# Kernel tuning notes

Hardware: AMD Instinct MI355X
Metric: run time of the kernel (lower is better)

The kernel has to match this reference:

```python
import jax, jax.numpy as jnp
import numpy as np

B, S, N, U, A = 256, 24, 207, 64, 256
H = N * U  # hidden_state_size = num_nodes * rnn_units


def setup_inputs() -> dict:
    key = jax.random.key(0)
    ks = jax.random.split(key, 9)
    return {
        "inputs": jax.random.normal(ks[0], (B, N), dtype=jnp.float32),
        "encoder_outputs": jax.random.normal(ks[1], (S, B, H), dtype=jnp.float32),
        "hidden_state": jax.random.normal(ks[2], (1, B, H), dtype=jnp.float32) * 0.05,
        "adj": jax.random.uniform(ks[3], (N, N), dtype=jnp.float32) / N,
        "attn_W": jax.random.normal(ks[4], (2 * H, A), dtype=jnp.float32) * 0.01,
        "attn_b": jnp.zeros((A,), dtype=jnp.float32),
        "attn_v": jax.random.normal(ks[5], (A,), dtype=jnp.float32) * 0.1,
        "W_ru": jax.random.normal(ks[6], (1 + 2 * U, 2 * U), dtype=jnp.float32) * 0.1,
        "b_ru": jnp.zeros((2 * U,), dtype=jnp.float32),
        "W_c": jax.random.normal(ks[7], (1 + 2 * U, U), dtype=jnp.float32) * 0.1,
        "b_c": jnp.zeros((U,), dtype=jnp.float32),
        "proj_W": jax.random.normal(ks[8], (2 * U + 1, 1), dtype=jnp.float32) * 0.1,
        "proj_b": jnp.zeros((1,), dtype=jnp.float32),
    }


def reference(inputs, encoder_outputs, hidden_state, adj, attn_W, attn_b, attn_v,
              W_ru, b_ru, W_c, b_c, proj_W, proj_b):
    b = inputs.shape[0]
    hid = hidden_state[-1]                               # (B, H) top-layer decoder state
    enc = jnp.transpose(encoder_outputs, (1, 0, 2))      # (B, S, H)

    # Bahdanau attention: tanh(Linear(cat(hid, enc))) . v, softmax over src_len.
    # Split the weight so we never materialize the (B, S, 2H) concat.
    Wh, We = attn_W[:H], attn_W[H:]
    energy = jnp.tanh((hid @ Wh)[:, None, :] + jnp.einsum('bsh,ha->bsa', enc, We) + attn_b)
    scores = energy @ attn_v                             # (B, S)
    a = jax.nn.softmax(scores, axis=1)
    weighted = jnp.einsum('bs,bsh->bh', a, enc).reshape(b, N, U)  # (B, N, U)

    # Graph-conv GRU cell (DCRNN-style), single layer.
    x = jnp.concatenate([inputs.reshape(b, N, 1), weighted], axis=-1)  # (B, N, 1+U)
    h = hid.reshape(b, N, U)
    m = jnp.einsum('nm,bmf->bnf', adj, jnp.concatenate([x, h], axis=-1))  # message passing
    ru = jax.nn.sigmoid(m @ W_ru + b_ru)                 # (B, N, 2U)
    r, u = ru[..., :U], ru[..., U:]
    mc = jnp.einsum('nm,bmf->bnf', adj, jnp.concatenate([x, r * h], axis=-1))
    c = jnp.tanh(mc @ W_c + b_c)                         # (B, N, U)
    new_h = u * h + (1.0 - u) * c                        # (B, N, U)

    # Projection: Linear(2U+1 -> 1) on per-node cat(output, weighted, inputs).
    proj_in = jnp.concatenate([new_h, weighted, inputs.reshape(b, N, 1)], axis=-1)
    output = (proj_in @ proj_W + proj_b).reshape(b, N)   # (B, N*output_dim)
    return output, new_h.reshape(1, b, H)
```

## Files before the change

kernel.cpp:

```cpp
#include <hip/hip_runtime.h>
#include <hip/hip_bf16.h>
#include <math.h>

#define B_ 256
#define S_ 24
#define N_ 207
#define U_ 64
#define A_ 256
#define H_ (N_*U_)
#define H2_ (2*H_)
#define BS_ (B_*S_)
#define NF_ 129
#define FP_ 192
#define KP_ 256
#define MR_ 6400
#define ZSPL_ 9

typedef __attribute__((ext_vector_type(8))) short bf16x8;
typedef __attribute__((ext_vector_type(4))) float f32x4;

#define GAS __attribute__((address_space(1)))
#define LAS __attribute__((address_space(3)))

static __device__ __forceinline__ void gload16(const __hip_bfloat16* g, void* lds) {
    __builtin_amdgcn_global_load_lds((const GAS uint32_t*)g, (LAS uint32_t*)lds, 16, 0, 0);
}

template<int BM, int BN, int EPI>
__global__ __launch_bounds__(256)
void mfma_gemm(const __hip_bfloat16* __restrict__ A, int lda,
               const __hip_bfloat16* __restrict__ BT, int ldb,
               void* __restrict__ Cv, int ldc,
               int kchunk, int niter,
               const float* __restrict__ ep0,
               const float* __restrict__ ep1,
               const float* __restrict__ ep2,
               const float* __restrict__ e_wt,
               const float* __restrict__ e_pw,
               const float* __restrict__ e_pb,
               const float* __restrict__ e_in,
               float* __restrict__ e_o0)
{
    constexpr int FM = BM / 32, FN = BN / 32;
    __shared__ __align__(128) char smem[(BM + BN) * 128];
    char* As = smem;
    char* Bs = smem + BM * 128;

    const int tid  = threadIdx.x;
    const int lane = tid & 63;
    const int wid  = tid >> 6;
    const int wr   = wid >> 1, wc = wid & 1;

    const int n0 = blockIdx.x * BN;
    const int m0 = blockIdx.y * BM;
    const long k0 = (long)blockIdx.z * kchunk;

    const int qk = lane >> 4;
    const int fr = lane & 15;
    const int sw = (lane & 7) << 4;

    f32x4 acc[FM][FN] = {};

    for (int it = 0; it < niter; ++it) {
        const long kb = k0 + (long)it * 64;
        #pragma unroll
        for (int p = 0; p < BM / 32; ++p) {
            const int chunk = p * 4 + wid;
            const int blk   = chunk * 64 + lane;
            const int r     = blk >> 3;
            const int klog  = ((blk & 7) << 4) ^ ((r & 7) << 4);
            gload16(A + (size_t)(m0 + r) * lda + kb + (klog >> 1), As + chunk * 1024);
        }
        #pragma unroll
        for (int p = 0; p < BN / 32; ++p) {
            const int chunk = p * 4 + wid;
            const int blk   = chunk * 64 + lane;
            const int r     = blk >> 3;
            const int klog  = ((blk & 7) << 4) ^ ((r & 7) << 4);
            gload16(BT + (size_t)(n0 + r) * ldb + kb + (klog >> 1), Bs + chunk * 1024);
        }
        __syncthreads();
        #pragma unroll
        for (int ks = 0; ks < 2; ++ks) {
            const int ko = ks * 64 + qk * 16;
            bf16x8 a[FM], b[FN];
            #pragma unroll
            for (int i = 0; i < FM; ++i)
                a[i] = *(const bf16x8*)(As + (wr * (BM/2) + i * 16 + fr) * 128 + (ko ^ sw));
            #pragma unroll
            for (int j = 0; j < FN; ++j)
                b[j] = *(const bf16x8*)(Bs + (wc * (BN/2) + j * 16 + fr) * 128 + (ko ^ sw));
            #pragma unroll
            for (int i = 0; i < FM; ++i)
                #pragma unroll
                for (int j = 0; j < FN; ++j)
                    acc[i][j] = __builtin_amdgcn_mfma_f32_16x16x32_bf16(a[i], b[j], acc[i][j], 0, 0, 0);
        }
        __syncthreads();
    }

    float* rsum = (float*)smem;
    if (EPI == 5) {
        if (tid < BM) rsum[tid] = 0.f;
        __syncthreads();
    }
    float tpart[FM][4];
    if (EPI == 5) {
        #pragma unroll
        for (int mi = 0; mi < FM; ++mi)
            #pragma unroll
            for (int q = 0; q < 4; ++q) tpart[mi][q] = 0.f;
    }

    #pragma unroll
    for (int mi = 0; mi < FM; ++mi)
        #pragma unroll
        for (int ni = 0; ni < FN; ++ni) {
            const int rbase = m0 + wr * (BM/2) + mi * 16 + qk * 4;
            const int col   = n0 + wc * (BN/2) + ni * 16 + fr;
            #pragma unroll
            for (int q = 0; q < 4; ++q) {
                const int row = rbase + q;
                const float v = acc[mi][ni][q];
                if (EPI == 2) {
                    ((__hip_bfloat16*)Cv)[(size_t)row * ldc + col] = __float2bfloat16(v);
                } else if (EPI == 3) {
                    const int bb = col >> 6, uu = col & 63;
                    ((__hip_bfloat16*)Cv)[((size_t)row * 256 + bb) * FP_ + 65 + uu] = __float2bfloat16(v);
                } else if (EPI == 4) {
                    float sv = v + ep0[col];
                    ((float*)Cv)[(size_t)row * ldc + col] = 1.f / (1.f + expf(-sv));
                } else {
                    const int nn = row >> 8, bb = row & 255;
                    float cg = tanhf(v + ep0[col]);
                    float ug = ep1[(size_t)row * 128 + 64 + col];
                    const size_t hoff = (size_t)bb * H_ + nn * U_ + col;
                    float nh = ug * ep2[hoff] + (1.f - ug) * cg;
                    ((float*)Cv)[hoff] = nh;
                    tpart[mi][q] += nh * e_pw[col] + e_wt[hoff] * e_pw[64 + col];
                }
            }
        }

    if (EPI == 5) {
        #pragma unroll
        for (int mi = 0; mi < FM; ++mi)
            #pragma unroll
            for (int q = 0; q < 4; ++q) {
                float t = tpart[mi][q];
                #pragma unroll
                for (int off = 8; off; off >>= 1) t += __shfl_xor(t, off, 16);
                if (fr == 0) {
                    const int rloc = wr * (BM/2) + mi * 16 + qk * 4 + q;
                    atomicAdd(&rsum[rloc], t);
                }
            }
        __syncthreads();
        if (tid < BM) {
            const int row = m0 + tid;
            const int nn = row >> 8, bb = row & 255;
            e_o0[bb * N_ + nn] = rsum[tid] + e_in[bb * N_ + nn] * e_pw[128] + e_pb[0];
        }
    }
}

__global__ __launch_bounds__(256)
void gemm_enchid(const float* __restrict__ Aenc,
                 const float* __restrict__ Ahid,
                 const __hip_bfloat16* __restrict__ WTBF,
                 float* __restrict__ Pz,
                 int kchunk, int niter)
{
    __shared__ __align__(128) char smem[(64 + 256) * 128];
    char* As = smem;
    char* Bs = smem + 64*128;

    const int tid  = threadIdx.x;
    const int lane = tid & 63;
    const int wid  = tid >> 6;
    const int wr   = wid >> 1, wc = wid & 1;

    const bool isH = (blockIdx.y >= 96);
    const float* A = isH ? Ahid : Aenc;
    const int lm0  = (isH ? (blockIdx.y - 96) : blockIdx.y) * 64;
    const int gm0  = (isH ? 6144 : 0) + lm0;
    const __hip_bfloat16* BT = WTBF + (isH ? 0 : H_);

    const long k0 = (long)blockIdx.z * kchunk;

    const int qk = lane >> 4;
    const int fr = lane & 15;
    const int sw = (lane & 7) << 4;

    f32x4 acc[2][8] = {};

    for (int it = 0; it < niter; ++it) {
        const long kb = k0 + (long)it * 64;
        #pragma unroll
        for (int h = 0; h < 2; ++h) {
            const int c  = h * 256 + tid;
            const int r  = c >> 3;
            const int kc = c & 7;
            const float* src = A + (size_t)(lm0 + r) * H_ + kb + kc * 8;
            const float4 x = *(const float4*)(src);
            const float4 y = *(const float4*)(src + 4);
            union { __hip_bfloat16 hh[8]; int4 u; } pk;
            pk.hh[0] = __float2bfloat16(x.x); pk.hh[1] = __float2bfloat16(x.y);
            pk.hh[2] = __float2bfloat16(x.z); pk.hh[3] = __float2bfloat16(x.w);
            pk.hh[4] = __float2bfloat16(y.x); pk.hh[5] = __float2bfloat16(y.y);
            pk.hh[6] = __float2bfloat16(y.z); pk.hh[7] = __float2bfloat16(y.w);
            *(int4*)(As + r * 128 + ((kc << 4) ^ ((r & 7) << 4))) = pk.u;
        }
        #pragma unroll
        for (int p = 0; p < 8; ++p) {
            const int chunk = p * 4 + wid;
            const int blk   = chunk * 64 + lane;
            const int r     = blk >> 3;
            const int klog  = ((blk & 7) << 4) ^ ((r & 7) << 4);
            gload16(BT + (size_t)r * H2_ + kb + (klog >> 1), Bs + chunk * 1024);
        }
        __syncthreads();
        #pragma unroll
        for (int ks = 0; ks < 2; ++ks) {
            const int ko = ks * 64 + qk * 16;
            bf16x8 a[2], b[8];
            #pragma unroll
            for (int i = 0; i < 2; ++i)
                a[i] = *(const bf16x8*)(As + (wr * 32 + i * 16 + fr) * 128 + (ko ^ sw));
            #pragma unroll
            for (int j = 0; j < 8; ++j)
                b[j] = *(const bf16x8*)(Bs + (wc * 128 + j * 16 + fr) * 128 + (ko ^ sw));
            #pragma unroll
            for (int i = 0; i < 2; ++i)
                #pragma unroll
                for (int j = 0; j < 8; ++j)
                    acc[i][j] = __builtin_amdgcn_mfma_f32_16x16x32_bf16(a[i], b[j], acc[i][j], 0, 0, 0);
        }
        __syncthreads();
    }

    float* Pzs = Pz + (size_t)blockIdx.z * MR_ * A_;
    #pragma unroll
    for (int mi = 0; mi < 2; ++mi)
        #pragma unroll
        for (int ni = 0; ni < 8; ++ni) {
            const int rbase = gm0 + wr * 32 + mi * 16 + qk * 4;
            const int col   = wc * 128 + ni * 16 + fr;
            #pragma unroll
            for (int q = 0; q < 4; ++q)
                Pzs[(size_t)(rbase + q) * A_ + col] = acc[mi][ni][q];
        }
}

__global__ __launch_bounds__(256)
void transpose_cvt_kernel(const float* __restrict__ in, __hip_bfloat16* __restrict__ out) {
    __shared__ float tile[32][33];
    const int h0 = blockIdx.x * 32, a0 = blockIdx.y * 32;
    const int tx = threadIdx.x & 31, ty4 = threadIdx.x >> 5;
    #pragma unroll
    for (int i = 0; i < 4; ++i) {
        int r = ty4 * 4 + i;
        tile[r][tx] = in[(size_t)(h0 + r) * A_ + a0 + tx];
    }
    __syncthreads();
    #pragma unroll
    for (int i = 0; i < 4; ++i) {
        int r = ty4 * 4 + i;
        out[(size_t)(a0 + r) * H2_ + h0 + tx] = __float2bfloat16(tile[tx][r]);
    }
}

__global__ __launch_bounds__(256)
void t1red_kernel(const float* __restrict__ Pz, const float* __restrict__ ab,
                  float* __restrict__ T1) {
    int i = blockIdx.x * 256 + threadIdx.x;
    int b = i >> 8, a = i & 255;
    float v = ab[a];
    #pragma unroll
    for (int z = 0; z < ZSPL_; ++z)
        v += Pz[((size_t)z * MR_ + 6144 + b) * A_ + a];
    T1[i] = v;
}

__global__ __launch_bounds__(256)
void scores_kernel(const float* __restrict__ Pz, const float* __restrict__ T1,
                   const float* __restrict__ v, float* __restrict__ SC) {
    int wave = threadIdx.x >> 6, lane = threadIdx.x & 63;
    int q = blockIdx.x * 4 + wave;
    if (q >= BS_) return;
    int b = q & 255;
    float s = 0.f;
    #pragma unroll
    for (int a = lane; a < A_; a += 64) {
        float val = T1[b * A_ + a];
        #pragma unroll
        for (int z = 0; z < ZSPL_; ++z)
            val += Pz[((size_t)z * MR_ + q) * A_ + a];
        s += tanhf(val) * v[a];
    }
    #pragma unroll
    for (int off = 32; off; off >>= 1) s += __shfl_down(s, off, 64);
    if (lane == 0) SC[q] = s;
}

__global__ __launch_bounds__(256)
void weighted_f32_kernel(const float4* __restrict__ E4, const float* __restrict__ SC,
                         float4* __restrict__ WT4) {
    int g = blockIdx.x * 256 + threadIdx.x;
    int b = g / (H_ / 4), c = g % (H_ / 4);
    float sc[S_];
    float mx = -1e30f;
    #pragma unroll
    for (int s = 0; s < S_; ++s) { sc[s] = SC[s * B_ + b]; mx = fmaxf(mx, sc[s]); }
    float sum = 0.f;
    #pragma unroll
    for (int s = 0; s < S_; ++s) { sc[s] = expf(sc[s] - mx); sum += sc[s]; }
    float inv = 1.f / sum;
    float4 acc = make_float4(0.f, 0.f, 0.f, 0.f);
    #pragma unroll
    for (int s = 0; s < S_; ++s) {
        float w = sc[s] * inv;
        float4 ev = E4[(size_t)(s * B_ + b) * (H_ / 4) + c];
        acc.x += w * ev.x; acc.y += w * ev.y;
        acc.z += w * ev.z; acc.w += w * ev.w;
    }
    WT4[(size_t)b * (H_ / 4) + c] = acc;
}

__global__ __launch_bounds__(256)
void catT_prepB_kernel(const float* __restrict__ inp, const float* __restrict__ WT,
                       const float* __restrict__ hid, __hip_bfloat16* __restrict__ CT,
                       const float* __restrict__ adj, const float* __restrict__ Wru,
                       const float* __restrict__ Wc, __hip_bfloat16* __restrict__ ADJ,
                       __hip_bfloat16* __restrict__ WRUT, __hip_bfloat16* __restrict__ WCT) {
    const int tid = threadIdx.x;
    if (blockIdx.y == 4) {
        for (int i = blockIdx.x * 256 + tid; i < 102400; i += 65536) {
            if (i < 65536) {
                int r = i >> 8, c = i & 255;
                ADJ[i] = __float2bfloat16((r < N_ && c < N_) ? adj[r * N_ + c] : 0.f);
            } else if (i < 90112) {
                int idx = i - 65536;
                int j = idx / FP_, f = idx % FP_;
                WRUT[idx] = __float2bfloat16(f < NF_ ? Wru[f * 128 + j] : 0.f);
            } else {
                int idx = i - 90112;
                int j = idx / FP_, f = idx % FP_;
                WCT[idx] = __float2bfloat16(f < NF_ ? Wc[f * 64 + j] : 0.f);
            }
        }
        return;
    }
    __shared__ float ww[64][65];
    __shared__ float wh[64][65];
    __shared__ float wi[64];
    const int b = blockIdx.x;
    const int k0 = blockIdx.y * 64;
    #pragma unroll
    for (int i = 0; i < 16; ++i) {
        int idx = tid + i * 256;
        int kn = idx >> 6, f = idx & 63;
        int k = k0 + kn;
        bool vld = (k < N_);
        ww[kn][f] = vld ? WT [(size_t)b * H_ + k * 64 + f] : 0.f;
        wh[kn][f] = vld ? hid[(size_t)b * H_ + k * 64 + f] : 0.f;
    }
    if (tid < 64) wi[tid] = (k0 + tid < N_) ? inp[b * N_ + k0 + tid] : 0.f;
    __syncthreads();
    #pragma unroll
    for (int i = 0; i < 6; ++i) {
        int cid = tid + i * 256;
        int f = cid >> 3, kk = (cid & 7) * 8;
        union { __hip_bfloat16 h[8]; bf16x8 v; } pk;
        #pragma unroll
        for (int j = 0; j < 8; ++j) {
            float x;
            if (f == 0)        x = wi[kk + j];
            else if (f <= 64)  x = ww[kk + j][f - 1];
            else if (f <= 128) x = wh[kk + j][f - 65];
            else               x = 0.f;
            pk.h[j] = __float2bfloat16(x);
        }
        *(bf16x8*)(CT + ((size_t)b * FP_ + f) * KP_ + k0 + kk) = pk.v;
    }
}

__global__ __launch_bounds__(256)
void rhT_kernel(const float* __restrict__ RU, const float* __restrict__ hid,
                __hip_bfloat16* __restrict__ RT) {
    __shared__ float rh[64][65];
    const int b = blockIdx.x, k0 = blockIdx.y * 64, tid = threadIdx.x;
    #pragma unroll
    for (int i = 0; i < 16; ++i) {
        int idx = tid + i * 256;
        int kn = idx >> 6, u = idx & 63;
        int k = k0 + kn;
        float v = 0.f;
        if (k < N_)
            v = RU[((size_t)k * 256 + b) * 128 + u] * hid[(size_t)b * H_ + k * 64 + u];
        rh[kn][u] = v;
    }
    __syncthreads();
    #pragma unroll
    for (int i = 0; i < 2; ++i) {
        int cid = tid + i * 256;
        int u = cid >> 3, kk = (cid & 7) * 8;
        union { __hip_bfloat16 h[8]; bf16x8 v; } pk;
        #pragma unroll
        for (int j = 0; j < 8; ++j) pk.h[j] = __float2bfloat16(rh[kk + j][u]);
        *(bf16x8*)(RT + ((size_t)b * 64 + u) * KP_ + k0 + kk) = pk.v;
    }
}

extern "C" void kernel_launch(void* const* d_in, const int* in_sizes, int n_in,
                              void* d_out, int out_size, void* d_ws, size_t ws_size,
                              hipStream_t stream) {
    const float* inp    = (const float*)d_in[0];
    const float* enc    = (const float*)d_in[1];
    const float* hid    = (const float*)d_in[2];
    const float* adj    = (const float*)d_in[3];
    const float* attn_W = (const float*)d_in[4];
    const float* attn_b = (const float*)d_in[5];
    const float* attn_v = (const float*)d_in[6];
    const float* W_ru   = (const float*)d_in[7];
    const float* b_ru   = (const float*)d_in[8];
    const float* W_c    = (const float*)d_in[9];
    const float* b_c    = (const float*)d_in[10];
    const float* proj_W = (const float*)d_in[11];
    const float* proj_b = (const float*)d_in[12];

    float* out0 = (float*)d_out;
    float* out2 = out0 + (size_t)B_ * N_;

    float* ws  = (float*)d_ws;
    float* T1  = ws;
    float* Pold= T1 + 65536;
    float* SC  = Pold + 1572864;
    float* AW  = SC + 6144;
    float* WT  = AW + 6144;
    float* BIG = WT + 3391488;
    float* Pz  = BIG;
    __hip_bfloat16* WT_BF  = (__hip_bfloat16*)(BIG + 40697856);
    __hip_bfloat16* CAT_T  = (__hip_bfloat16*)BIG;
    __hip_bfloat16* MB_BF  = (__hip_bfloat16*)(BIG + 6291456);
    __hip_bfloat16* RH_T   = (__hip_bfloat16*)(BIG + 12582912);
    float*          RU     = BIG + 14680064;
    __hip_bfloat16* ADJ_BF = (__hip_bfloat16*)(BIG + 21463040);
    __hip_bfloat16* WRUT   = (__hip_bfloat16*)(BIG + 21495808);
    __hip_bfloat16* WCT    = (__hip_bfloat16*)(BIG + 21508096);

    transpose_cvt_kernel<<<dim3(H2_/32, A_/32), 256, 0, stream>>>(attn_W, WT_BF);

    gemm_enchid<<<dim3(1, 100, ZSPL_), 256, 0, stream>>>(
        enc, hid, WT_BF, Pz, 1472, 23);

    t1red_kernel<<<256, 256, 0, stream>>>(Pz, attn_b, T1);
    scores_kernel<<<BS_/4, 256, 0, stream>>>(Pz, T1, attn_v, SC);
    weighted_f32_kernel<<<(B_*(H_/4))/256, 256, 0, stream>>>(
        (const float4*)enc, SC, (float4*)WT);

    catT_prepB_kernel<<<dim3(256, 5), 256, 0, stream>>>(
        inp, WT, hid, CAT_T, adj, W_ru, W_c, ADJ_BF, WRUT, WCT);

    mfma_gemm<64,64,2><<<dim3(768,4,1), 256, 0, stream>>>(
        ADJ_BF, KP_, CAT_T, KP_, MB_BF, 49152, 0, 4,
        nullptr, nullptr, nullptr, nullptr, nullptr, nullptr, nullptr, nullptr);

    mfma_gemm<64,64,4><<<dim3(2,828,1), 256, 0, stream>>>(
        MB_BF, FP_, WRUT, FP_, RU, 128, 0, 3,
        b_ru, nullptr, nullptr, nullptr, nullptr, nullptr, nullptr, nullptr);

    rhT_kernel<<<dim3(256,4), 256, 0, stream>>>(RU, hid, RH_T);

    mfma_gemm<64,64,3><<<dim3(256,4,1), 256, 0, stream>>>(
        ADJ_BF, KP_, RH_T, KP_, MB_BF, 0, 0, 4,
        nullptr, nullptr, nullptr, nullptr, nullptr, nullptr, nullptr, nullptr);

    mfma_gemm<64,64,5><<<dim3(1,828,1), 256, 0, stream>>>(
        MB_BF, FP_, WCT, FP_, out2, 0, 0, 3,
        b_c, RU, hid, WT, proj_W, proj_b, inp, out0);
}
```

Measured before the change: 282.8 us.

## Double-buffer LDS tiles in enc/hid attention GEMM with register prefetch

Splits shared memory into two stages. The next K-tile of the bf16 weights is loaded asynchronously into the alternate buffer, and the next fp32 activation chunk is prefetched into registers while MFMAs run on the current buffer. It also removes one barrier per iteration. The cost is double the LDS (80KB per block), which may lower occupancy, and higher register pressure from the prefetched float4s.

```diff
diff --git a/kernel.cpp b/kernel.cpp
--- a/kernel.cpp
+++ b/kernel.cpp
@@ -171,9 +171,7 @@
                  float* __restrict__ Pz,
                  int kchunk, int niter)
 {
-    __shared__ __align__(128) char smem[(64 + 256) * 128];
-    char* As = smem;
-    char* Bs = smem + 64*128;
+    __shared__ __align__(128) char smem[2 * (64 + 256) * 128];
 
     const int tid  = threadIdx.x;
     const int lane = tid & 63;
@@ -192,51 +190,99 @@
     const int fr = lane & 15;
     const int sw = (lane & 7) << 4;
 
+    int arow[2], akc[2];
+    #pragma unroll
+    for (int h = 0; h < 2; ++h) {
+        const int c = h * 256 + tid;
+        arow[h] = c >> 3;
+        akc[h]  = c & 7;
+    }
+
     f32x4 acc[2][8] = {};
-
-    for (int it = 0; it < niter; ++it) {
-        const long kb = k0 + (long)it * 64;
-        #pragma unroll
-        for (int h = 0; h < 2; ++h) {
-            const int c  = h * 256 + tid;
-            const int r  = c >> 3;
-            const int kc = c & 7;
-            const float* src = A + (size_t)(lm0 + r) * H_ + kb + kc * 8;
-            const float4 x = *(const float4*)(src);
-            const float4 y = *(const float4*)(src + 4);
-            union { __hip_bfloat16 hh[8]; int4 u; } pk;
-            pk.hh[0] = __float2bfloat16(x.x); pk.hh[1] = __float2bfloat16(x.y);
-            pk.hh[2] = __float2bfloat16(x.z); pk.hh[3] = __float2bfloat16(x.w);
-            pk.hh[4] = __float2bfloat16(y.x); pk.hh[5] = __float2bfloat16(y.y);
-            pk.hh[6] = __float2bfloat16(y.z); pk.hh[7] = __float2bfloat16(y.w);
-            *(int4*)(As + r * 128 + ((kc << 4) ^ ((r & 7) << 4))) = pk.u;
-        }
+    float4 pfx[2], pfy[2];
+
+    {
+        const long kb = k0;
         #pragma unroll
         for (int p = 0; p < 8; ++p) {
             const int chunk = p * 4 + wid;
             const int blk   = chunk * 64 + lane;
             const int r     = blk >> 3;
             const int klog  = ((blk & 7) << 4) ^ ((r & 7) << 4);
-            gload16(BT + (size_t)r * H2_ + kb + (klog >> 1), Bs + chunk * 1024);
+            gload16(BT + (size_t)r * H2_ + kb + (klog >> 1), smem + 8192 + chunk * 1024);
+        }
+        #pragma unroll
+        for (int h = 0; h < 2; ++h) {
+            const float* src = A + (size_t)(lm0 + arow[h]) * H_ + kb + akc[h] * 8;
+            pfx[h] = *(const float4*)(src);
+            pfy[h] = *(const float4*)(src + 4);
+        }
+        #pragma unroll
+        for (int h = 0; h < 2; ++h) {
+            union { __hip_bfloat16 hh[8]; int4 u; } pk;
+            pk.hh[0] = __float2bfloat16(pfx[h].x); pk.hh[1] = __float2bfloat16(pfx[h].y);
+            pk.hh[2] = __float2bfloat16(pfx[h].z); pk.hh[3] = __float2bfloat16(pfx[h].w);
+            pk.hh[4] = __float2bfloat16(pfy[h].x); pk.hh[5] = __float2bfloat16(pfy[h].y);
+            pk.hh[6] = __float2bfloat16(pfy[h].z); pk.hh[7] = __float2bfloat16(pfy[h].w);
+            *(int4*)(smem + arow[h] * 128 + ((akc[h] << 4) ^ ((arow[h] & 7) << 4))) = pk.u;
         }
         __syncthreads();
+    }
+
+    int cur = 0;
+    for (int it = 0; it < niter; ++it) {
+        char* curbuf = smem + cur * 40960;
+        char* altbuf = smem + (cur ^ 1) * 40960;
+        const bool pf = (it + 1 < niter);
+        const long kbn = k0 + (long)(it + 1) * 64;
+
+        if (pf) {
+            #pragma unroll
+            for (int p = 0; p < 8; ++p) {
+                const int chunk = p * 4 + wid;
+                const int blk   = chunk * 64 + lane;
+                const int r     = blk >> 3;
+                const int klog  = ((blk & 7) << 4) ^ ((r & 7) << 4);
+                gload16(BT + (size_t)r * H2_ + kbn + (klog >> 1), altbuf + 8192 + chunk * 1024);
+            }
+            #pragma unroll
+            for (int h = 0; h < 2; ++h) {
+                const float* src = A + (size_t)(lm0 + arow[h]) * H_ + kbn + akc[h] * 8;
+                pfx[h] = *(const float4*)(src);
+                pfy[h] = *(const float4*)(src + 4);
+            }
+        }
+
         #pragma unroll
         for (int ks = 0; ks < 2; ++ks) {
             const int ko = ks * 64 + qk * 16;
             bf16x8 a[2], b[8];
             #pragma unroll
             for (int i = 0; i < 2; ++i)
-                a[i] = *(const bf16x8*)(As + (wr * 32 + i * 16 + fr) * 128 + (ko ^ sw));
+                a[i] = *(const bf16x8*)(curbuf + (wr * 32 + i * 16 + fr) * 128 + (ko ^ sw));
             #pragma unroll
             for (int j = 0; j < 8; ++j)
-                b[j] = *(const bf16x8*)(Bs + (wc * 128 + j * 16 + fr) * 128 + (ko ^ sw));
+                b[j] = *(const bf16x8*)(curbuf + 8192 + (wc * 128 + j * 16 + fr) * 128 + (ko ^ sw));
             #pragma unroll
             for (int i = 0; i < 2; ++i)
                 #pragma unroll
                 for (int j = 0; j < 8; ++j)
                     acc[i][j] = __builtin_amdgcn_mfma_f32_16x16x32_bf16(a[i], b[j], acc[i][j], 0, 0, 0);
         }
+
+        if (pf) {
+            #pragma unroll
+            for (int h = 0; h < 2; ++h) {
+                union { __hip_bfloat16 hh[8]; int4 u; } pk;
+                pk.hh[0] = __float2bfloat16(pfx[h].x); pk.hh[1] = __float2bfloat16(pfx[h].y);
+                pk.hh[2] = __float2bfloat16(pfx[h].z); pk.hh[3] = __float2bfloat16(pfx[h].w);
+                pk.hh[4] = __float2bfloat16(pfy[h].x); pk.hh[5] = __float2bfloat16(pfy[h].y);
+                pk.hh[6] = __float2bfloat16(pfy[h].z); pk.hh[7] = __float2bfloat16(pfy[h].w);
+                *(int4*)(altbuf + arow[h] * 128 + ((akc[h] << 4) ^ ((arow[h] & 7) << 4))) = pk.u;
+            }
+        }
         __syncthreads();
+        cur ^= 1;
     }
 
     float* Pzs = Pz + (size_t)blockIdx.z * MR_ * A_;
```

After: 265.1 us (median of 2 runs). 6.2% less time.
